# Kernel tuning notes

Hardware: AMD Instinct MI355X
Metric: run time of the kernel (lower is better)

The kernel has to match this reference:

```python
import jax, jax.numpy as jnp
import numpy as np

B, S, E, H = 4, 4096, 768, 8
D = E // H  # head_dim = 96


def setup_inputs() -> dict:
    key = jax.random.key(0)
    ks = jax.random.split(key, 9)
    std = 1.0 / np.sqrt(E)
    return {
        "values": jax.random.normal(ks[0], (B, S, E), dtype=jnp.float32),
        "keys": jax.random.normal(ks[1], (B, S, E), dtype=jnp.float32),
        "query": jax.random.normal(ks[2], (B, S, E), dtype=jnp.float32),
        "mask": jax.random.randint(ks[3], (B, S, 1, 1), 0, 2, dtype=jnp.int32),
        "Wv": jax.random.normal(ks[4], (E, E), dtype=jnp.float32) * std,
        "Wk": jax.random.normal(ks[5], (E, E), dtype=jnp.float32) * std,
        "Wq": jax.random.normal(ks[6], (E, E), dtype=jnp.float32) * std,
        "Wo": jax.random.normal(ks[7], (E, E), dtype=jnp.float32) * std,
        "bo": jax.random.normal(ks[8], (E,), dtype=jnp.float32) * std,
    }


def reference(values, keys, query, mask, Wv, Wk, Wq, Wo, bo):
    b, s, e = query.shape
    h, d = H, e // H
    scale = e ** 0.5

    def split(x, W):
        # Linear (no bias) then view to [b, s, h, d] and permute to [b, h, s, d]
        return (x @ W.T).reshape(b, s, h, d).transpose(0, 2, 1, 3)

    v = split(values, Wv)   # [b, h, s, d]
    k = split(keys, Wk)     # [b, h, s, d]
    q = split(query, Wq)    # [b, h, s, d]

    # Faithful to torch.einsum('nqhd,nkhd->nhqk', q, k) with q,k laid out as
    # [b, h, s, d]: this contracts over d with s batched, producing a per-token
    # head-gram matrix att[b, s, i, j] = sum_d q[b,i,s,d] * k[b,j,s,d].
    att = jnp.einsum('bisd,bjsd->bsij', q, k)          # [b, s, h, h]
    att = jnp.where(mask == 0, jnp.float32(-1e20), att)
    att = jax.nn.softmax(att / scale, axis=3)

    # torch.einsum('nhql,nlhd->nqhd', att, v) with att [b,s,h,h], v [b,h,s,d]:
    # out[b, i, s, d] = sum_j att[b,s,i,j] * v[b,j,s,d]  -> [b, h, s, d]
    out = jnp.einsum('bsij,bjsd->bisd', att, v)        # [b, h, s, d]
    out = out.reshape(b, s, h * d)                      # row-major, matches torch .reshape
    return out @ Wo.T + bo
```

## Files before the change

kernel.cpp:

```cpp
#include <hip/hip_runtime.h>
#include <hip/hip_bf16.h>
#include <cstdint>


typedef unsigned short u16;
typedef short bf16x8 __attribute__((ext_vector_type(8)));
typedef float f32x4 __attribute__((ext_vector_type(4)));

#define B_  4
#define S_  4096
#define E_  768
#define H_  8
#define D_  96
#define T_  (B_*S_)
#define BM_ 128
#define BN_ 128
#define NT_ (E_/BN_)

static __device__ __forceinline__ u16 f2bf(float f) {
  unsigned u = __builtin_bit_cast(unsigned, f);
  u += 0x7fffu + ((u >> 16) & 1u);
  return (u16)(u >> 16);
}
static __device__ __forceinline__ unsigned pk2(float lo, float hi) {
  return (unsigned)f2bf(lo) | ((unsigned)f2bf(hi) << 16);
}
static __device__ __forceinline__ float bflo(unsigned u) {
  return __builtin_bit_cast(float, u << 16);
}
static __device__ __forceinline__ float bfhi(unsigned u) {
  return __builtin_bit_cast(float, u & 0xffff0000u);
}

__global__ __launch_bounds__(256) void conv_w(
    const float* __restrict__ w0, const float* __restrict__ w1,
    const float* __restrict__ w2, const float* __restrict__ w3,
    u16* __restrict__ dst)
{
  const int bpw = (E_ * E_ / 4) / 256;
  const int which = blockIdx.x / bpw;
  const float* src = which == 0 ? w0 : which == 1 ? w1 : which == 2 ? w2 : w3;
  const int i = (blockIdx.x - which * bpw) * 256 + threadIdx.x;
  const float4 v = ((const float4*)src)[i];
  uint2 w;
  w.x = pk2(v.x, v.y);
  w.y = pk2(v.z, v.w);
  ((uint2*)(dst + (size_t)which * E_ * E_))[i] = w;
}

__global__ __launch_bounds__(256) void conv3(
    const float* __restrict__ q, const float* __restrict__ k,
    const float* __restrict__ v, u16* __restrict__ xq,
    u16* __restrict__ xk, u16* __restrict__ xv)
{
  const int w = blockIdx.y;
  const float* src = w == 0 ? q : w == 1 ? k : v;
  u16* dst = w == 0 ? xq : w == 1 ? xk : xv;
  const int i = blockIdx.x * 256 + threadIdx.x;
  const float4 vv = ((const float4*)src)[i];
  uint2 o;
  o.x = pk2(vv.x, vv.y);
  o.y = pk2(vv.z, vv.w);
  ((uint2*)dst)[i] = o;
}


#define GLOAD(SRC, DST)                                                        \
  __builtin_amdgcn_global_load_lds(                                            \
      (const __attribute__((address_space(1))) void*)(SRC),                    \
      (__attribute__((address_space(3))) void*)(DST), 16, 0, 0)

#define STAGE(BUF, KT)                                                         \
  {                                                                            \
    _Pragma("unroll")                                                          \
    for (int c = 0; c < 2; ++c) {                                              \
      const int idx = (c << 8) + tid;                                          \
      const int r = idx >> 2, g = idx & 3;                                     \
      const int gs = g ^ ((r >> 1) & 3);                                       \
      GLOAD(A + (size_t)(tM + r) * E_ + (KT) + (gs << 3),                      \
            &lds[BUF][0][((c << 8) + (wave << 6)) << 3]);                      \
      GLOAD(Wt + (size_t)(tN + r) * E_ + (KT) + (gs << 3),                     \
            &lds[BUF][1][((c << 8) + (wave << 6)) << 3]);                      \
    }                                                                          \
  }

#define LOADFRAGS(BUF)                                                         \
  {                                                                            \
    _Pragma("unroll")                                                          \
    for (int m = 0; m < 4; ++m)                                                \
      a[m] = *(const bf16x8*)&lds[BUF][0][(((wr << 6) + (m << 4) + l15) << 5) + slotOff]; \
    _Pragma("unroll")                                                          \
    for (int n = 0; n < 4; ++n)                                                \
      b[n] = *(const bf16x8*)&lds[BUF][1][(((wc << 6) + (n << 4) + l15) << 5) + slotOff]; \
  }

#define DOMFMA()                                                               \
  {                                                                            \
    _Pragma("unroll")                                                          \
    for (int m = 0; m < 4; ++m)                                                \
      _Pragma("unroll")                                                        \
      for (int n = 0; n < 4; ++n)                                              \
        acc[m][n] = __builtin_amdgcn_mfma_f32_16x16x32_bf16(a[m], b[n], acc[m][n], 0, 0, 0); \
  }

#define STEP(RB, SB, KT, STG, VM)                                              \
  {                                                                            \
    bf16x8 a[4], b[4];                                                         \
    LOADFRAGS(RB);                                                             \
    if (STG) STAGE(SB, KT);                                                    \
    DOMFMA();                                                                  \
    asm volatile("s_waitcnt vmcnt(" #VM ")\n\ts_barrier" ::: "memory");        \
  }

template<bool BATCHED, bool OUT_F32, bool BIAS>
__global__ __launch_bounds__(256, 3) void gemm_nt(
    const u16* __restrict__ a0, const u16* __restrict__ a1,
    const u16* __restrict__ a2, const u16* __restrict__ Wall,
    const float* __restrict__ bias,
    void* __restrict__ c0, void* __restrict__ c1, void* __restrict__ c2)
{
  __shared__ u16 lds[3][2][4096];
  const u16* A;
  const u16* Wt;
  void* Cv;
  if constexpr (BATCHED) {
    const int q_ = blockIdx.y;
    A  = q_ == 0 ? a0 : q_ == 1 ? a1 : a2;
    Wt = Wall + (size_t)q_ * (E_ * E_);
    Cv = q_ == 0 ? c0 : q_ == 1 ? c1 : c2;
  } else {
    A = a0; Wt = Wall; Cv = c0;
  }

  {
    int sidx = blockIdx.x >> 8;
    if constexpr (BATCHED) sidx = (sidx + blockIdx.y) % 3;
#pragma unroll 1
    for (int z = 0; z < sidx; ++z) __builtin_amdgcn_s_sleep(3);
  }

  const int tid  = threadIdx.x;
  const int wave = tid >> 6;
  const int lane = tid & 63;
  const int wr = wave >> 1, wc = wave & 1;
  const int bid = blockIdx.x;
  const int wg  = (bid & 7) * 96 + (bid >> 3);
  const int mT  = wg / NT_;
  const int nT  = wg - mT * NT_;
  const int tM = mT * BM_, tN = nT * BN_;
  const int l15 = lane & 15, l4 = lane >> 4;
  const int slotOff = (l4 ^ ((l15 >> 1) & 3)) << 3;

  f32x4 acc[4][4] = {};

  STAGE(0, 0);
  STAGE(1, 32);
  asm volatile("s_waitcnt vmcnt(4)\n\ts_barrier" ::: "memory");

#pragma unroll 1
  for (int it = 0; it < 7; ++it) {
    const int kt = it * 96;
    STEP(0, 2, kt + 64,  true, 4);
    STEP(1, 0, kt + 96,  true, 4);
    STEP(2, 1, kt + 128, true, 4);
  }
  STEP(0, 2, 736, true, 4);
  STEP(1, 0, 0,   false, 0);
  {
    bf16x8 a[4], b[4];
    LOADFRAGS(2);
    DOMFMA();
  }

  if constexpr (OUT_F32) {
#pragma unroll
    for (int m = 0; m < 4; ++m) {
#pragma unroll
      for (int n = 0; n < 4; ++n) {
        const int row = tM + (wr << 6) + (m << 4) + (l4 << 2);
        const int col = tN + (wc << 6) + (n << 4) + l15;
        const float badd = BIAS ? bias[col] : 0.f;
#pragma unroll
        for (int r = 0; r < 4; ++r)
          ((float*)Cv)[(size_t)(row + r) * E_ + col] = acc[m][n][r] + badd;
      }
    }
  } else {
    __syncthreads();
    u16* lC = (u16*)lds;
#pragma unroll
    for (int m = 0; m < 4; ++m)
#pragma unroll
      for (int n = 0; n < 4; ++n) {
        const int row = (wr << 6) + (m << 4) + (l4 << 2);
        const int col = (wc << 6) + (n << 4) + l15;
#pragma unroll
        for (int r = 0; r < 4; ++r)
          lC[(row + r) * BN_ + col] = f2bf(acc[m][n][r]);
      }
    __syncthreads();
#pragma unroll
    for (int p = 0; p < 8; ++p) {
      const int row = (p << 4) + (wave << 2) + l4;
      const bf16x8 v = *(const bf16x8*)&lC[row * BN_ + (l15 << 3)];
      *(bf16x8*)((u16*)Cv + (size_t)(tM + row) * E_ + tN + (l15 << 3)) = v;
    }
  }
}

__global__ __launch_bounds__(256) void attn_tok(
    const u16* __restrict__ Q, const u16* __restrict__ K,
    const u16* __restrict__ V, const int* __restrict__ mask,
    u16* __restrict__ O)
{
  __shared__ float pl[4][8][8];
  const int tid = threadIdx.x, wave = tid >> 6, lane = tid & 63;
  const int t = blockIdx.x * 4 + wave;
  const int s = t & (S_ - 1);
  const int b = t >> 12;
  const int i = lane >> 3, j = lane & 7;

  const uint4* qp = (const uint4*)(Q + (size_t)t * E_ + i * D_);
  const uint4* kp = (const uint4*)(K + (size_t)t * E_ + j * D_);
  float acc = 0.f;
#pragma unroll
  for (int it = 0; it < 12; ++it) {
    const uint4 qv = qp[it], kv = kp[it];
    acc += bflo(qv.x) * bflo(kv.x) + bfhi(qv.x) * bfhi(kv.x);
    acc += bflo(qv.y) * bflo(kv.y) + bfhi(qv.y) * bfhi(kv.y);
    acc += bflo(qv.z) * bflo(kv.z) + bfhi(qv.z) * bfhi(kv.z);
    acc += bflo(qv.w) * bflo(kv.w) + bfhi(qv.w) * bfhi(kv.w);
  }
  float sv = (mask[t] == 0) ? -1e20f : acc;
  sv *= 0.03608439182435161f;
  float mx = sv;
  mx = fmaxf(mx, __shfl_xor(mx, 1));
  mx = fmaxf(mx, __shfl_xor(mx, 2));
  mx = fmaxf(mx, __shfl_xor(mx, 4));
  const float e = __expf(sv - mx);
  float sm = e;
  sm += __shfl_xor(sm, 1);
  sm += __shfl_xor(sm, 2);
  sm += __shfl_xor(sm, 4);
  pl[wave][i][j] = e / sm;
  __syncthreads();

  const int i2 = lane >> 3, db = lane & 7;
  float o[12] = {};
#pragma unroll
  for (int jj = 0; jj < 8; ++jj) {
    const float pj = pl[wave][i2][jj];
    const uint2* vp = (const uint2*)(V + (size_t)t * E_ + jj * D_ + db * 12);
    const uint2 v0 = vp[0], v1 = vp[1], v2 = vp[2];
    o[0]  += pj * bflo(v0.x);  o[1]  += pj * bfhi(v0.x);
    o[2]  += pj * bflo(v0.y);  o[3]  += pj * bfhi(v0.y);
    o[4]  += pj * bflo(v1.x);  o[5]  += pj * bfhi(v1.x);
    o[6]  += pj * bflo(v1.y);  o[7]  += pj * bfhi(v1.y);
    o[8]  += pj * bflo(v2.x);  o[9]  += pj * bfhi(v2.x);
    o[10] += pj * bflo(v2.y);  o[11] += pj * bfhi(v2.y);
  }
  const size_t row = (size_t)b * S_ + 512 * i2 + (s >> 3);
  u16* op = O + row * E_ + 96 * (s & 7) + db * 12;
  uint2 w0, w1, w2;
  w0.x = pk2(o[0], o[1]);
  w0.y = pk2(o[2], o[3]);
  w1.x = pk2(o[4], o[5]);
  w1.y = pk2(o[6], o[7]);
  w2.x = pk2(o[8], o[9]);
  w2.y = pk2(o[10], o[11]);
  ((uint2*)op)[0] = w0;
  ((uint2*)op)[1] = w1;
  ((uint2*)op)[2] = w2;
}

extern "C" void kernel_launch(void* const* d_in, const int* in_sizes, int n_in,
                              void* d_out, int out_size, void* d_ws, size_t ws_size,
                              hipStream_t stream)
{
  const float* values = (const float*)d_in[0];
  const float* keys   = (const float*)d_in[1];
  const float* query  = (const float*)d_in[2];
  const int*   mask   = (const int*)d_in[3];
  const float* Wv = (const float*)d_in[4];
  const float* Wk = (const float*)d_in[5];
  const float* Wq = (const float*)d_in[6];
  const float* Wo = (const float*)d_in[7];
  const float* bo = (const float*)d_in[8];

  const size_t TE = (size_t)T_ * E_;
  const size_t EE = (size_t)E_ * E_;
  u16* Qb = (u16*)d_ws;
  u16* Kb = Qb + TE;
  u16* Vb = Kb + TE;
  u16* Xq = Vb + TE;
  u16* Wb = Xq + TE;
  u16* Xk = (u16*)d_out;
  u16* Xv = Xk + TE;

  dim3 blk(256);

  conv_w<<<dim3(4 * (E_ * E_ / 4) / 256), blk, 0, stream>>>(Wq, Wk, Wv, Wo, Wb);

  conv3<<<dim3(TE / 4 / 256, 3), blk, 0, stream>>>(query, keys, values, Xq, Xk, Xv);

  gemm_nt<true, false, false><<<dim3(T_ / BM_ * NT_, 3), blk, 0, stream>>>(
      Xq, Xk, Xv, Wb, nullptr, Qb, Kb, Vb);

  attn_tok<<<dim3(T_ / 4), blk, 0, stream>>>(Qb, Kb, Vb, mask, Xq );

  gemm_nt<false, true, true><<<dim3(T_ / BM_ * NT_), blk, 0, stream>>>(
      Xq , nullptr, nullptr, Wb + 3 * EE, bo, (float*)d_out, nullptr, nullptr);
}
```

Measured before the change: 169.0 us.

## Stage GEMM tiles into wave-private LDS regions to drop per-step barriers

Each wave now loads its own 64 rows of A and 64 rows of W into a private LDS slice, so the K-loop only needs s_waitcnt and no workgroup s_barrier. The sleep-based block stagger is removed and launch bounds drop to one block per CU, since LDS use doubles to 96KB. The cost is duplicated global/L2 traffic, because waves sharing a row or column tile each fetch it, plus lower occupancy and less latency hiding.

```diff
diff --git a/kernel.cpp b/kernel.cpp
--- a/kernel.cpp
+++ b/kernel.cpp
@@ -70,28 +70,30 @@
       (const __attribute__((address_space(1))) void*)(SRC),                    \
       (__attribute__((address_space(3))) void*)(DST), 16, 0, 0)
 
+#define RBASE(BUF, AB) ((((BUF) * 4 + wave) * 2 + (AB)) * 2048)
+
 #define STAGE(BUF, KT)                                                         \
   {                                                                            \
     _Pragma("unroll")                                                          \
-    for (int c = 0; c < 2; ++c) {                                              \
-      const int idx = (c << 8) + tid;                                          \
-      const int r = idx >> 2, g = idx & 3;                                     \
-      const int gs = g ^ ((r >> 1) & 3);                                       \
-      GLOAD(A + (size_t)(tM + r) * E_ + (KT) + (gs << 3),                      \
-            &lds[BUF][0][((c << 8) + (wave << 6)) << 3]);                      \
-      GLOAD(Wt + (size_t)(tN + r) * E_ + (KT) + (gs << 3),                     \
-            &lds[BUF][1][((c << 8) + (wave << 6)) << 3]);                      \
+    for (int c = 0; c < 4; ++c) {                                              \
+      const int rl = (c << 4) + (lane >> 2);                                   \
+      const int gs = (lane & 3) ^ ((rl >> 1) & 3);                             \
+      GLOAD(A + (size_t)(tM + (wr << 6) + rl) * E_ + (KT) + (gs << 3),         \
+            &lds[RBASE(BUF, 0) + (c << 9)]);                                   \
+      GLOAD(Wt + (size_t)(tN + (wc << 6) + rl) * E_ + (KT) + (gs << 3),        \
+            &lds[RBASE(BUF, 1) + (c << 9)]);                                   \
     }                                                                          \
   }
 
 #define LOADFRAGS(BUF)                                                         \
   {                                                                            \
     _Pragma("unroll")                                                          \
-    for (int m = 0; m < 4; ++m)                                                \
-      a[m] = *(const bf16x8*)&lds[BUF][0][(((wr << 6) + (m << 4) + l15) << 5) + slotOff]; \
-    _Pragma("unroll")                                                          \
-    for (int n = 0; n < 4; ++n)                                                \
-      b[n] = *(const bf16x8*)&lds[BUF][1][(((wc << 6) + (n << 4) + l15) << 5) + slotOff]; \
+    for (int m = 0; m < 4; ++m) {                                              \
+      const int r = (m << 4) + l15;                                            \
+      const int so = (l4 ^ ((r >> 1) & 3)) << 3;                               \
+      a[m] = *(const bf16x8*)&lds[RBASE(BUF, 0) + (r << 5) + so];              \
+      b[m] = *(const bf16x8*)&lds[RBASE(BUF, 1) + (r << 5) + so];              \
+    }                                                                          \
   }
 
 #define DOMFMA()                                                               \
@@ -103,23 +105,23 @@
         acc[m][n] = __builtin_amdgcn_mfma_f32_16x16x32_bf16(a[m], b[n], acc[m][n], 0, 0, 0); \
   }
 
-#define STEP(RB, SB, KT, STG, VM)                                              \
+#define STEP(RB, SB, KTS, STG, VM)                                             \
   {                                                                            \
+    asm volatile("s_waitcnt vmcnt(" #VM ")" ::: "memory");                     \
     bf16x8 a[4], b[4];                                                         \
     LOADFRAGS(RB);                                                             \
-    if (STG) STAGE(SB, KT);                                                    \
+    if (STG) STAGE(SB, KTS);                                                   \
     DOMFMA();                                                                  \
-    asm volatile("s_waitcnt vmcnt(" #VM ")\n\ts_barrier" ::: "memory");        \
   }
 
 template<bool BATCHED, bool OUT_F32, bool BIAS>
-__global__ __launch_bounds__(256, 3) void gemm_nt(
+__global__ __launch_bounds__(256, 1) void gemm_nt(
     const u16* __restrict__ a0, const u16* __restrict__ a1,
     const u16* __restrict__ a2, const u16* __restrict__ Wall,
     const float* __restrict__ bias,
     void* __restrict__ c0, void* __restrict__ c1, void* __restrict__ c2)
 {
-  __shared__ u16 lds[3][2][4096];
+  __shared__ u16 lds[49152];
   const u16* A;
   const u16* Wt;
   void* Cv;
@@ -132,13 +134,6 @@
     A = a0; Wt = Wall; Cv = c0;
   }
 
-  {
-    int sidx = blockIdx.x >> 8;
-    if constexpr (BATCHED) sidx = (sidx + blockIdx.y) % 3;
-#pragma unroll 1
-    for (int z = 0; z < sidx; ++z) __builtin_amdgcn_s_sleep(3);
-  }
-
   const int tid  = threadIdx.x;
   const int wave = tid >> 6;
   const int lane = tid & 63;
@@ -149,28 +144,22 @@
   const int nT  = wg - mT * NT_;
   const int tM = mT * BM_, tN = nT * BN_;
   const int l15 = lane & 15, l4 = lane >> 4;
-  const int slotOff = (l4 ^ ((l15 >> 1) & 3)) << 3;
 
   f32x4 acc[4][4] = {};
 
   STAGE(0, 0);
   STAGE(1, 32);
-  asm volatile("s_waitcnt vmcnt(4)\n\ts_barrier" ::: "memory");
 
 #pragma unroll 1
   for (int it = 0; it < 7; ++it) {
     const int kt = it * 96;
-    STEP(0, 2, kt + 64,  true, 4);
-    STEP(1, 0, kt + 96,  true, 4);
-    STEP(2, 1, kt + 128, true, 4);
-  }
-  STEP(0, 2, 736, true, 4);
-  STEP(1, 0, 0,   false, 0);
-  {
-    bf16x8 a[4], b[4];
-    LOADFRAGS(2);
-    DOMFMA();
-  }
+    STEP(0, 2, kt + 64,  true, 8);
+    STEP(1, 0, kt + 96,  true, 8);
+    STEP(2, 1, kt + 128, true, 8);
+  }
+  STEP(0, 2, 736, true, 8);
+  STEP(1, 0, 0,   false, 8);
+  STEP(2, 0, 0,   false, 0);
 
   if constexpr (OUT_F32) {
 #pragma unroll
@@ -187,7 +176,7 @@
     }
   } else {
     __syncthreads();
-    u16* lC = (u16*)lds;
+    u16* lC = lds;
 #pragma unroll
     for (int m = 0; m < 4; ++m)
 #pragma unroll
```

After: 202.7 us. +19.9%, slower.

## Load GEMM B fragments directly from global into registers, halving LDS

Applied to the files above, without the earlier changes.

The GEMM no longer stages the weight (B) tile through LDS. Each wave loads its B fragments straight from global memory into double-buffered registers one k-step ahead, while A is still triple-buffered in LDS via global_load_lds. This halves LDS usage (24KB instead of 48KB), which may raise occupancy and cut LDS traffic. The bf16 epilogue is reworked to write the output tile in two halves so it fits the smaller LDS. The cost is uncoalesced per-lane 16-byte global loads of weights, and more register pressure from the extra fragment buffers.

```diff
diff --git a/kernel.cpp b/kernel.cpp
--- a/kernel.cpp
+++ b/kernel.cpp
@@ -70,7 +70,7 @@
       (const __attribute__((address_space(1))) void*)(SRC),                    \
       (__attribute__((address_space(3))) void*)(DST), 16, 0, 0)
 
-#define STAGE(BUF, KT)                                                         \
+#define STAGE_A(BUF, KT)                                                       \
   {                                                                            \
     _Pragma("unroll")                                                          \
     for (int c = 0; c < 2; ++c) {                                              \
@@ -78,38 +78,44 @@
       const int r = idx >> 2, g = idx & 3;                                     \
       const int gs = g ^ ((r >> 1) & 3);                                       \
       GLOAD(A + (size_t)(tM + r) * E_ + (KT) + (gs << 3),                      \
-            &lds[BUF][0][((c << 8) + (wave << 6)) << 3]);                      \
-      GLOAD(Wt + (size_t)(tN + r) * E_ + (KT) + (gs << 3),                     \
-            &lds[BUF][1][((c << 8) + (wave << 6)) << 3]);                      \
+            &lds[(BUF) * 4096 + (((c << 8) + (wave << 6)) << 3)]);             \
     }                                                                          \
   }
 
-#define LOADFRAGS(BUF)                                                         \
+#define LOADFRAGS_A(BUF)                                                       \
   {                                                                            \
     _Pragma("unroll")                                                          \
     for (int m = 0; m < 4; ++m)                                                \
-      a[m] = *(const bf16x8*)&lds[BUF][0][(((wr << 6) + (m << 4) + l15) << 5) + slotOff]; \
+      a[m] = *(const bf16x8*)&lds[(BUF) * 4096 +                               \
+                 (((wr << 6) + (m << 4) + l15) << 5) + slotOff];               \
+  }
+
+#define LOADB(DST, KT)                                                         \
+  {                                                                            \
     _Pragma("unroll")                                                          \
     for (int n = 0; n < 4; ++n)                                                \
-      b[n] = *(const bf16x8*)&lds[BUF][1][(((wc << 6) + (n << 4) + l15) << 5) + slotOff]; \
-  }
-
-#define DOMFMA()                                                               \
+      DST[n] = __builtin_bit_cast(bf16x8,                                      \
+          *(const uint4*)(wbase + (size_t)(n << 4) * E_ + (KT)));              \
+  }
+
+#define DOMFMA(BV)                                                             \
   {                                                                            \
     _Pragma("unroll")                                                          \
     for (int m = 0; m < 4; ++m)                                                \
       _Pragma("unroll")                                                        \
       for (int n = 0; n < 4; ++n)                                              \
-        acc[m][n] = __builtin_amdgcn_mfma_f32_16x16x32_bf16(a[m], b[n], acc[m][n], 0, 0, 0); \
-  }
-
-#define STEP(RB, SB, KT, STG, VM)                                              \
-  {                                                                            \
-    bf16x8 a[4], b[4];                                                         \
-    LOADFRAGS(RB);                                                             \
-    if (STG) STAGE(SB, KT);                                                    \
-    DOMFMA();                                                                  \
-    asm volatile("s_waitcnt vmcnt(" #VM ")\n\ts_barrier" ::: "memory");        \
+        acc[m][n] = __builtin_amdgcn_mfma_f32_16x16x32_bf16(a[m], BV[n], acc[m][n], 0, 0, 0); \
+  }
+
+#define STEP(RB, SB, KTS, STG, BC, BNX, KTB, LB, VM)                           \
+  {                                                                            \
+    asm volatile("s_waitcnt vmcnt(" #VM ")" ::: "memory");                     \
+    __builtin_amdgcn_s_barrier();                                              \
+    bf16x8 a[4];                                                               \
+    LOADFRAGS_A(RB);                                                           \
+    if (LB) LOADB(BNX, KTB);                                                   \
+    if (STG) STAGE_A(SB, KTS);                                                 \
+    DOMFMA(BC);                                                                \
   }
 
 template<bool BATCHED, bool OUT_F32, bool BIAS>
@@ -119,7 +125,7 @@
     const float* __restrict__ bias,
     void* __restrict__ c0, void* __restrict__ c1, void* __restrict__ c2)
 {
-  __shared__ u16 lds[3][2][4096];
+  __shared__ u16 lds[3 * 4096];
   const u16* A;
   const u16* Wt;
   void* Cv;
@@ -150,27 +156,33 @@
   const int tM = mT * BM_, tN = nT * BN_;
   const int l15 = lane & 15, l4 = lane >> 4;
   const int slotOff = (l4 ^ ((l15 >> 1) & 3)) << 3;
+  const u16* wbase = Wt + (size_t)(tN + (wc << 6) + l15) * E_ + (l4 << 3);
 
   f32x4 acc[4][4] = {};
-
-  STAGE(0, 0);
-  STAGE(1, 32);
-  asm volatile("s_waitcnt vmcnt(4)\n\ts_barrier" ::: "memory");
+  bf16x8 bE[4], bO[4];
+
+  STAGE_A(0, 0);
+  LOADB(bE, 0);
+  STAGE_A(1, 32);
+  asm volatile("s_waitcnt vmcnt(2)" ::: "memory");
+  __builtin_amdgcn_s_barrier();
 
 #pragma unroll 1
-  for (int it = 0; it < 7; ++it) {
-    const int kt = it * 96;
-    STEP(0, 2, kt + 64,  true, 4);
-    STEP(1, 0, kt + 96,  true, 4);
-    STEP(2, 1, kt + 128, true, 4);
-  }
-  STEP(0, 2, 736, true, 4);
-  STEP(1, 0, 0,   false, 0);
-  {
-    bf16x8 a[4], b[4];
-    LOADFRAGS(2);
-    DOMFMA();
-  }
+  for (int it = 0; it < 3; ++it) {
+    const int kb = it * 192;
+    STEP(0, 2, kb + 64,  1, bE, bO, kb + 32,  1, 2);
+    STEP(1, 0, kb + 96,  1, bO, bE, kb + 64,  1, 2);
+    STEP(2, 1, kb + 128, 1, bE, bO, kb + 96,  1, 2);
+    STEP(0, 2, kb + 160, 1, bO, bE, kb + 128, 1, 2);
+    STEP(1, 0, kb + 192, 1, bE, bO, kb + 160, 1, 2);
+    STEP(2, 1, kb + 224, 1, bO, bE, kb + 192, 1, 2);
+  }
+  STEP(0, 2, 640, 1, bE, bO, 608, 1, 2);
+  STEP(1, 0, 672, 1, bO, bE, 640, 1, 2);
+  STEP(2, 1, 704, 1, bE, bO, 672, 1, 2);
+  STEP(0, 2, 736, 1, bO, bE, 704, 1, 2);
+  STEP(1, 0, 0,   0, bE, bO, 736, 1, 2);
+  STEP(2, 0, 0,   0, bO, bO, 0,   0, 0);
 
   if constexpr (OUT_F32) {
 #pragma unroll
@@ -186,24 +198,30 @@
       }
     }
   } else {
-    __syncthreads();
-    u16* lC = (u16*)lds;
-#pragma unroll
-    for (int m = 0; m < 4; ++m)
-#pragma unroll
-      for (int n = 0; n < 4; ++n) {
-        const int row = (wr << 6) + (m << 4) + (l4 << 2);
-        const int col = (wc << 6) + (n << 4) + l15;
-#pragma unroll
-        for (int r = 0; r < 4; ++r)
-          lC[(row + r) * BN_ + col] = f2bf(acc[m][n][r]);
+    u16* lC = lds;
+#pragma unroll
+    for (int p = 0; p < 2; ++p) {
+      __syncthreads();
+      if (wr == p) {
+#pragma unroll
+        for (int m = 0; m < 4; ++m)
+#pragma unroll
+          for (int n = 0; n < 4; ++n) {
+            const int row = (m << 4) + (l4 << 2);
+            const int col = (wc << 6) + (n << 4) + l15;
+#pragma unroll
+            for (int r = 0; r < 4; ++r)
+              lC[(row + r) * BN_ + col] = f2bf(acc[m][n][r]);
+          }
       }
-    __syncthreads();
-#pragma unroll
-    for (int p = 0; p < 8; ++p) {
-      const int row = (p << 4) + (wave << 2) + l4;
-      const bf16x8 v = *(const bf16x8*)&lC[row * BN_ + (l15 << 3)];
-      *(bf16x8*)((u16*)Cv + (size_t)(tM + row) * E_ + tN + (l15 << 3)) = v;
+      __syncthreads();
+#pragma unroll
+      for (int itr = 0; itr < 4; ++itr) {
+        const int row16 = (itr << 4) + (tid >> 4);
+        const bf16x8 v = *(const bf16x8*)&lC[row16 * BN_ + ((tid & 15) << 3)];
+        *(bf16x8*)((u16*)Cv + (size_t)(tM + (p << 6) + row16) * E_ + tN +
+                   ((tid & 15) << 3)) = v;
+      }
     }
   }
 }
```

After: 237.2 us. +40.3%, slower.
